# Kernel tuning notes

Hardware: AMD Instinct MI355X
Metric: run time of the kernel (lower is better)

The kernel has to match this reference:

```python
import jax, jax.numpy as jnp
import numpy as np

NUM_HEADS = 8
MODEL_DIM = 1024
SEQ_LEN = 2048


def setup_inputs() -> dict:
    key = jax.random.key(0)
    ks = jax.random.split(key, 9)
    H, D, L = NUM_HEADS, MODEL_DIM, SEQ_LEN
    s_in = 1.0 / np.sqrt(D)
    s_out = 1.0 / np.sqrt(H * D)
    return {
        "tokens": jax.random.normal(ks[0], (D, L), dtype=jnp.float32),
        "Wq": jax.random.uniform(ks[1], (H * D, D), jnp.float32, -s_in, s_in),
        "bq": jax.random.uniform(ks[2], (H * D,), jnp.float32, -s_in, s_in),
        "Wk": jax.random.uniform(ks[3], (H * D, D), jnp.float32, -s_in, s_in),
        "bk": jax.random.uniform(ks[4], (H * D,), jnp.float32, -s_in, s_in),
        "Wv": jax.random.uniform(ks[5], (H * D, D), jnp.float32, -s_in, s_in),
        "bv": jax.random.uniform(ks[6], (H * D,), jnp.float32, -s_in, s_in),
        "Wo": jax.random.uniform(ks[7], (D, H * D), jnp.float32, -s_out, s_out),
        "bo": jax.random.uniform(ks[8], (D,), jnp.float32, -s_out, s_out),
    }


def _split_heads(x, H, D, L):
    # Faithful to torch: raw .view of contiguous [H*D, L] into (L, H, D),
    # then permute(1, 2, 0) -> (H, D, L). This is a memory reinterpretation,
    # not a transpose, exactly as in the original module.
    return x.reshape(L, H, D).transpose(1, 2, 0)


def reference(tokens, Wq, bq, Wk, bk, Wv, bv, Wo, bo):
    D, L = tokens.shape
    H = Wq.shape[0] // D
    # 1x1 Conv1d == matmul over channel dim
    q = _split_heads(Wq @ tokens + bq[:, None], H, D, L)  # (H, D, L)
    k = _split_heads(Wk @ tokens + bk[:, None], H, D, L)  # (H, D, L)
    v = _split_heads(Wv @ tokens + bv[:, None], H, D, L)  # (H, D, L)
    scores = jnp.einsum("hdl,hdm->hlm", q, k) / np.sqrt(D)  # (H, L, L)
    # torch F.softmax without dim on a 3D tensor -> dim=0 (head axis)
    attn = jax.nn.softmax(scores, axis=0)
    ctx = jnp.einsum("hlm,hdm->hdl", attn, v)  # (H, D, L)
    out = Wo @ ctx.reshape(H * D, L) + bo[:, None]  # (D, L)
    return out
```

## Files before the change

kernel.cpp:

```cpp
#include <hip/hip_runtime.h>

#define SEQL 2048
#define DMODEL 1024
#define HDIM 8192

typedef unsigned short bf16_t;
typedef __attribute__((ext_vector_type(8))) short bf16x8;
typedef __attribute__((ext_vector_type(4))) float f32x4;

__device__ __forceinline__ bf16_t f2bf(float f) {
  unsigned u = __float_as_uint(f);
  u += 0x7fffu + ((u >> 16) & 1u);
  return (bf16_t)(u >> 16);
}
__device__ __forceinline__ float bf2f(bf16_t b) {
  return __uint_as_float(((unsigned)b) << 16);
}

__global__ __launch_bounds__(256) void cvt_f32_bf16(const float* __restrict__ in,
                                                    bf16_t* __restrict__ out, int n) {
  int i = (blockIdx.x * 256 + threadIdx.x) * 4;
  if (i >= n) return;
  float4 f = *reinterpret_cast<const float4*>(in + i);
  ushort4 u;
  u.x = f2bf(f.x); u.y = f2bf(f.y); u.z = f2bf(f.z); u.w = f2bf(f.w);
  *reinterpret_cast<ushort4*>(out + i) = u;
}

__global__ __launch_bounds__(256) void transpose_cvt(const float* __restrict__ in,
                                                     bf16_t* __restrict__ out) {
  __shared__ float tile[32][33];
  int bx = blockIdx.x * 32;
  int by = blockIdx.y * 32;
  int tx = threadIdx.x, ty = threadIdx.y;
#pragma unroll
  for (int i = ty; i < 32; i += 8)
    tile[i][tx] = in[(size_t)(by + i) * SEQL + bx + tx];
  __syncthreads();
#pragma unroll
  for (int i = ty; i < 32; i += 8)
    out[(size_t)(bx + i) * DMODEL + by + tx] = f2bf(tile[tx][i]);
}

__global__ __launch_bounds__(256) void softmax_heads(bf16_t* __restrict__ S) {
  const size_t HS = (size_t)SEQL * SEQL;
  size_t p = ((size_t)blockIdx.x * 256 + threadIdx.x) * 8;
  float v[8][8];
#pragma unroll
  for (int h = 0; h < 8; ++h) {
    bf16x8 x = *reinterpret_cast<const bf16x8*>(S + h * HS + p);
#pragma unroll
    for (int e = 0; e < 8; ++e) v[h][e] = bf2f((bf16_t)x[e]);
  }
#pragma unroll
  for (int e = 0; e < 8; ++e) {
    float mx = v[0][e];
#pragma unroll
    for (int h = 1; h < 8; ++h) mx = fmaxf(mx, v[h][e]);
    float s = 0.f;
#pragma unroll
    for (int h = 0; h < 8; ++h) { v[h][e] = __expf(v[h][e] - mx); s += v[h][e]; }
    float inv = 1.0f / s;
#pragma unroll
    for (int h = 0; h < 8; ++h) v[h][e] *= inv;
  }
#pragma unroll
  for (int h = 0; h < 8; ++h) {
    bf16x8 x;
#pragma unroll
    for (int e = 0; e < 8; ++e) x[e] = (short)f2bf(v[h][e]);
    *reinterpret_cast<bf16x8*>(S + h * HS + p) = x;
  }
}

__global__ __launch_bounds__(256) void reduce_out(const float* __restrict__ P,
                                                  const float* __restrict__ bo,
                                                  float* __restrict__ out) {
  const size_t NEL = (size_t)DMODEL * SEQL;
  size_t i = ((size_t)blockIdx.x * 256 + threadIdx.x) * 4;
  float4 a = *reinterpret_cast<const float4*>(P + i);
#pragma unroll
  for (int z = 1; z < 8; ++z) {
    float4 b = *reinterpret_cast<const float4*>(P + z * NEL + i);
    a.x += b.x; a.y += b.y; a.z += b.z; a.w += b.w;
  }
  float bias = bo[i / SEQL];
  a.x += bias; a.y += bias; a.z += bias; a.w += bias;
  *reinterpret_cast<float4*>(out + i) = a;
}

template <typename OutT, int EPI, bool HAS_BIAS>
__global__ __launch_bounds__(512, 2) void gemm256(
    const bf16_t* __restrict__ A, const bf16_t* __restrict__ B,
    OutT* __restrict__ C, const float* __restrict__ bias,
    int M, int N, int K, int lda, int ldb, int ldc,
    long long sA, long long sB, long long sC, float scale, int gx) {
  __shared__ alignas(16) char smem[147456];
  auto* As = reinterpret_cast<bf16_t(*)[2][8192]>(smem);
  auto* Bs = reinterpret_cast<bf16_t(*)[2][8192]>(smem + 65536);
  const int z = blockIdx.z;
  A += (long long)z * sA;
  B += (long long)z * sB;
  C += (long long)z * sC;
  const int nwg = gridDim.x;
  const int bid = blockIdx.x;
  const int swz = (nwg & 7) ? bid : ((bid & 7) * (nwg >> 3) + (bid >> 3));
  const int brow = (swz / gx) * 256;
  const int bcol = (swz % gx) * 256;
  const int tid = threadIdx.x;
  const int w = tid >> 6, lane = tid & 63;
  const int fr = lane & 15, fq = lane >> 4;
  const int wr = w >> 2, wc = w & 3;

  int rj[2], cj[2];
#pragma unroll
  for (int j = 0; j < 2; ++j) {
    const int c = (w * 2 + j) * 64 + lane;
    rj[j] = c >> 3;
    cj[j] = ((c & 7) ^ (rj[j] & 7)) << 3;
  }

  auto stageA = [&](int buf, int half, int kk) {
#pragma unroll
    for (int j = 0; j < 2; ++j) {
      const bf16_t* g = A + (size_t)(brow + half * 128 + rj[j]) * lda + kk + cj[j];
      __builtin_amdgcn_global_load_lds(
          (const __attribute__((address_space(1))) void*)g,
          (__attribute__((address_space(3))) void*)(&As[buf][half][(w * 2 + j) * 512]),
          16, 0, 0);
    }
  };
  auto stageB = [&](int buf, int half, int kk) {
#pragma unroll
    for (int j = 0; j < 2; ++j) {
      const bf16_t* g = B + (size_t)(bcol + half * 128 + rj[j]) * ldb + kk + cj[j];
      __builtin_amdgcn_global_load_lds(
          (const __attribute__((address_space(1))) void*)g,
          (__attribute__((address_space(3))) void*)(&Bs[buf][half][(w * 2 + j) * 512]),
          16, 0, 0);
    }
  };

  auto ldA = [&](int buf, int mf, int kk) -> bf16x8 {
    const int rr = mf * 16 + fr;
    return *reinterpret_cast<const bf16x8*>(
        &As[buf][wr][rr * 64 + ((((kk << 2) | fq) ^ (rr & 7)) << 3)]);
  };
  auto ldB = [&](int buf, int nf, int kk) -> bf16x8 {
    const int rr = (wc & 1) * 64 + nf * 16 + fr;
    return *reinterpret_cast<const bf16x8*>(
        &Bs[buf][wc >> 1][rr * 64 + ((((kk << 2) | fq) ^ (rr & 7)) << 3)]);
  };

  f32x4 acc[8][4];
  const f32x4 fzero = {0.f, 0.f, 0.f, 0.f};
#pragma unroll
  for (int m = 0; m < 8; ++m)
#pragma unroll
    for (int n = 0; n < 4; ++n) acc[m][n] = fzero;

  const int NT = K >> 6;
  stageA(0, 0, 0); stageA(0, 1, 0); stageB(0, 0, 0); stageB(0, 1, 0);
  __syncthreads();

  for (int t = 0; t < NT; ++t) {
    const int p = t & 1, q = p ^ 1;
    const int kn = (t + 1) << 6;
    const bool pre = (t + 1 < NT);
    bf16x8 af[4][2], bg[4][2];

    if (pre) { stageA(q, 0, kn); stageA(q, 1, kn); }
#pragma unroll
    for (int mf = 0; mf < 4; ++mf)
#pragma unroll
      for (int kk = 0; kk < 2; ++kk) af[mf][kk] = ldA(p, mf, kk);
#pragma unroll
    for (int nf = 0; nf < 2; ++nf)
#pragma unroll
      for (int kk = 0; kk < 2; ++kk) bg[nf][kk] = ldB(p, nf, kk);
    __builtin_amdgcn_s_setprio(1);
#pragma unroll
    for (int mf = 0; mf < 4; ++mf)
#pragma unroll
      for (int nf = 0; nf < 2; ++nf)
#pragma unroll
        for (int kk = 0; kk < 2; ++kk)
          acc[mf][nf] = __builtin_amdgcn_mfma_f32_16x16x32_bf16(
              af[mf][kk], bg[nf][kk], acc[mf][nf], 0, 0, 0);
    __builtin_amdgcn_s_setprio(0);

    if (pre) { stageB(q, 0, kn); stageB(q, 1, kn); }
#pragma unroll
    for (int nf = 2; nf < 4; ++nf)
#pragma unroll
      for (int kk = 0; kk < 2; ++kk) bg[nf][kk] = ldB(p, nf, kk);
    __builtin_amdgcn_s_setprio(1);
#pragma unroll
    for (int mf = 0; mf < 4; ++mf)
#pragma unroll
      for (int nf = 2; nf < 4; ++nf)
#pragma unroll
        for (int kk = 0; kk < 2; ++kk)
          acc[mf][nf] = __builtin_amdgcn_mfma_f32_16x16x32_bf16(
              af[mf][kk], bg[nf][kk], acc[mf][nf], 0, 0, 0);
    __builtin_amdgcn_s_setprio(0);

#pragma unroll
    for (int mf = 0; mf < 4; ++mf)
#pragma unroll
      for (int kk = 0; kk < 2; ++kk) af[mf][kk] = ldA(p, mf + 4, kk);
    __builtin_amdgcn_s_setprio(1);
#pragma unroll
    for (int mf = 0; mf < 4; ++mf)
#pragma unroll
      for (int nf = 2; nf < 4; ++nf)
#pragma unroll
        for (int kk = 0; kk < 2; ++kk)
          acc[mf + 4][nf] = __builtin_amdgcn_mfma_f32_16x16x32_bf16(
              af[mf][kk], bg[nf][kk], acc[mf + 4][nf], 0, 0, 0);
    __builtin_amdgcn_s_setprio(0);

#pragma unroll
    for (int nf = 0; nf < 2; ++nf)
#pragma unroll
      for (int kk = 0; kk < 2; ++kk) bg[nf][kk] = ldB(p, nf, kk);
    __builtin_amdgcn_s_setprio(1);
#pragma unroll
    for (int mf = 0; mf < 4; ++mf)
#pragma unroll
      for (int nf = 0; nf < 2; ++nf)
#pragma unroll
        for (int kk = 0; kk < 2; ++kk)
          acc[mf + 4][nf] = __builtin_amdgcn_mfma_f32_16x16x32_bf16(
              af[mf][kk], bg[nf][kk], acc[mf + 4][nf], 0, 0, 0);
    __builtin_amdgcn_s_setprio(0);

    if (pre) __syncthreads();
  }

  __syncthreads();

  if constexpr (EPI == 0) {
    bf16_t* Ct = (bf16_t*)smem;
#pragma unroll
    for (int mf = 0; mf < 8; ++mf)
#pragma unroll
      for (int j = 0; j < 4; ++j) {
        const int orow = wr * 128 + mf * 16 + fq * 4 + j;
        float bvv = HAS_BIAS ? bias[brow + orow] : 0.f;
#pragma unroll
        for (int nf = 0; nf < 4; ++nf)
          Ct[orow * 264 + wc * 64 + nf * 16 + fr] = f2bf(acc[mf][nf][j] * scale + bvv);
      }
    __syncthreads();
#pragma unroll
    for (int i = 0; i < 16; ++i) {
      const int c = tid + i * 512;
      const int row = c >> 5, ch = c & 31;
      *reinterpret_cast<bf16x8*>(&C[(size_t)(brow + row) * ldc + bcol + ch * 8]) =
          *reinterpret_cast<const bf16x8*>(smem + row * 528 + ch * 16);
    }
  } else if constexpr (EPI == 1) {
    float* Cf = (float*)smem;
#pragma unroll
    for (int h = 0; h < 2; ++h) {
      if (wr == h) {
#pragma unroll
        for (int mf = 0; mf < 8; ++mf)
#pragma unroll
          for (int j = 0; j < 4; ++j) {
            const int orow = mf * 16 + fq * 4 + j;
            float bvv = HAS_BIAS ? bias[brow + h * 128 + orow] : 0.f;
#pragma unroll
            for (int nf = 0; nf < 4; ++nf)
              Cf[orow * 264 + wc * 64 + nf * 16 + fr] = acc[mf][nf][j] * scale + bvv;
          }
      }
      __syncthreads();
#pragma unroll
      for (int i = 0; i < 16; ++i) {
        const int c = tid + i * 512;
        const int row = c >> 6, ch = c & 63;
        *reinterpret_cast<float4*>(&C[(size_t)(brow + h * 128 + row) * ldc + bcol + ch * 4]) =
            *reinterpret_cast<const float4*>(smem + row * 1056 + ch * 16);
      }
      __syncthreads();
    }
  } else {
    bf16_t* Vt = (bf16_t*)smem;
#pragma unroll
    for (int mf = 0; mf < 8; ++mf)
#pragma unroll
      for (int j = 0; j < 4; ++j) {
        const int i = wr * 128 + mf * 16 + fq * 4 + j;
        const int mloc = i >> 2;
        float bvv = HAS_BIAS ? bias[brow + i] : 0.f;
#pragma unroll
        for (int nf = 0; nf < 4; ++nf) {
          const int dloc = wc * 64 + nf * 16 + fr;
          Vt[(j * 256 + dloc) * 72 + mloc] = f2bf(acc[mf][nf][j] * scale + bvv);
        }
      }
    __syncthreads();
    const int r_ = bcol >> 10, d0 = bcol & 1023, m0 = brow >> 2;
#pragma unroll
    for (int sIt = 0; sIt < 2; ++sIt) {
      const int s = tid + sIt * 512;
      const int h2 = s >> 8, dloc = s & 255;
      const bf16_t* src = Vt + (h2 * 256 + dloc) * 72;
      bf16_t* dst = (bf16_t*)C + ((size_t)(2 * h2 + r_) * DMODEL + d0 + dloc) * SEQL + m0;
#pragma unroll
      for (int qq = 0; qq < 8; ++qq)
        *reinterpret_cast<bf16x8*>(dst + qq * 8) =
            *reinterpret_cast<const bf16x8*>(src + qq * 8);
    }
  }
}

extern "C" void kernel_launch(void* const* d_in, const int* in_sizes, int n_in,
                              void* d_out, int out_size, void* d_ws, size_t ws_size,
                              hipStream_t stream) {
  const float* tokens = (const float*)d_in[0];
  const float* Wq = (const float*)d_in[1];
  const float* bq = (const float*)d_in[2];
  const float* Wk = (const float*)d_in[3];
  const float* bk = (const float*)d_in[4];
  const float* Wv = (const float*)d_in[5];
  const float* bv = (const float*)d_in[6];
  const float* Wo = (const float*)d_in[7];
  const float* bo = (const float*)d_in[8];
  float* out = (float*)d_out;
  char* ws = (char*)d_ws;
  const size_t MB = 1024ull * 1024ull;
  bf16_t* tT = (bf16_t*)(ws + 0);
  bf16_t* Wb = (bf16_t*)(ws + 4 * MB);
  bf16_t* Qm = (bf16_t*)(ws + 20 * MB);
  bf16_t* Km = (bf16_t*)(ws + 52 * MB);
  bf16_t* Vs = (bf16_t*)(ws + 84 * MB);
  bf16_t* Sb = (bf16_t*)(ws + 116 * MB);
  bf16_t* cT = (bf16_t*)(ws + 20 * MB);
  float* Pp = (float*)(ws + 116 * MB);

  dim3 b256(256);
  dim3 b512(512);
  const int nW = HDIM * DMODEL;

  transpose_cvt<<<dim3(SEQL / 32, DMODEL / 32), dim3(32, 8), 0, stream>>>(tokens, tT);

  cvt_f32_bf16<<<nW / 1024, b256, 0, stream>>>(Wq, Wb, nW);
  gemm256<bf16_t, 0, true><<<dim3(32 * 8, 1, 1), b512, 0, stream>>>(
      Wb, tT, Qm, bq, HDIM, SEQL, DMODEL, DMODEL, DMODEL, SEQL, 0, 0, 0, 1.0f, 8);
  cvt_f32_bf16<<<nW / 1024, b256, 0, stream>>>(Wk, Wb, nW);
  gemm256<bf16_t, 0, true><<<dim3(32 * 8, 1, 1), b512, 0, stream>>>(
      Wb, tT, Km, bk, HDIM, SEQL, DMODEL, DMODEL, DMODEL, SEQL, 0, 0, 0, 1.0f, 8);
  cvt_f32_bf16<<<nW / 1024, b256, 0, stream>>>(Wv, Wb, nW);
  gemm256<bf16_t, 2, true><<<dim3(32 * 8, 1, 1), b512, 0, stream>>>(
      Wb, tT, Vs, bv, HDIM, SEQL, DMODEL, DMODEL, DMODEL, SEQL, 0, 0, 0, 1.0f, 8);

  gemm256<bf16_t, 0, false><<<dim3(8 * 8, 1, 8), b512, 0, stream>>>(
      Qm, Km, Sb, nullptr, SEQL, SEQL, DMODEL, HDIM, HDIM, SEQL,
      1024, 1024, (long long)SEQL * SEQL, 0.03125f, 8);

  softmax_heads<<<(SEQL * SEQL / 8) / 256, b256, 0, stream>>>(Sb);

  gemm256<bf16_t, 0, false><<<dim3(8 * 4, 1, 8), b512, 0, stream>>>(
      Sb, Vs, cT, nullptr, SEQL, DMODEL, SEQL, SEQL, SEQL, HDIM,
      (long long)SEQL * SEQL, (long long)DMODEL * SEQL, DMODEL, 1.0f, 4);

  cvt_f32_bf16<<<nW / 1024, b256, 0, stream>>>(Wo, Wb, nW);
  gemm256<float, 1, false><<<dim3(4 * 8, 1, 8), b512, 0, stream>>>(
      Wb, cT, Pp, nullptr, DMODEL, SEQL, 1024, HDIM, HDIM, SEQL,
      1024, 1024, (long long)DMODEL * SEQL, 1.0f, 8);
  reduce_out<<<(DMODEL * SEQL / 4) / 256, b256, 0, stream>>>(Pp, bo, out);
}
```

Measured before the change: 369.2 us.

## Fuse Q/K/V projections into one GEMM and flatten batched grids

Converts Wq, Wk and Wv into one concatenated bf16 weight buffer and runs a single 768-tile GEMM that writes Q and K row-major and V in its transposed-split layout, chosen per tile. All batched GEMMs now fold the batch index into a flat 1D grid, so the XCD swizzle covers every tile instead of only one z-slice. The intent is to cut launch count, fill the GPU better with more tiles per launch, and reduce per-launch tail effects. The cost is larger workspace and a runtime branch in the epilogue.

```diff
diff --git a/kernel.cpp b/kernel.cpp
--- a/kernel.cpp
+++ b/kernel.cpp
@@ -27,6 +27,32 @@
   *reinterpret_cast<ushort4*>(out + i) = u;
 }
 
+__global__ __launch_bounds__(256) void cvt3_f32_bf16(const float* __restrict__ a,
+                                                     const float* __restrict__ b,
+                                                     const float* __restrict__ c,
+                                                     bf16_t* __restrict__ out) {
+  const int SEG = HDIM * DMODEL;
+  int i = (blockIdx.x * 256 + threadIdx.x) * 4;
+  const float* src;
+  int off;
+  if (i < SEG) { src = a; off = i; }
+  else if (i < 2 * SEG) { src = b; off = i - SEG; }
+  else { src = c; off = i - 2 * SEG; }
+  float4 f = *reinterpret_cast<const float4*>(src + off);
+  ushort4 u;
+  u.x = f2bf(f.x); u.y = f2bf(f.y); u.z = f2bf(f.z); u.w = f2bf(f.w);
+  *reinterpret_cast<ushort4*>(out + i) = u;
+}
+
+__global__ __launch_bounds__(256) void bias3(const float* __restrict__ a,
+                                             const float* __restrict__ b,
+                                             const float* __restrict__ c,
+                                             float* __restrict__ out) {
+  int i = blockIdx.x * 256 + threadIdx.x;
+  float v = (i < HDIM) ? a[i] : (i < 2 * HDIM) ? b[i - HDIM] : c[i - 2 * HDIM];
+  out[i] = v;
+}
+
 __global__ __launch_bounds__(256) void transpose_cvt(const float* __restrict__ in,
                                                      bf16_t* __restrict__ out) {
   __shared__ float tile[32][33];
@@ -92,21 +118,22 @@
 template <typename OutT, int EPI, bool HAS_BIAS>
 __global__ __launch_bounds__(512, 2) void gemm256(
     const bf16_t* __restrict__ A, const bf16_t* __restrict__ B,
-    OutT* __restrict__ C, const float* __restrict__ bias,
-    int M, int N, int K, int lda, int ldb, int ldc,
-    long long sA, long long sB, long long sC, float scale, int gx) {
+    OutT* __restrict__ C, bf16_t* __restrict__ C2, const float* __restrict__ bias,
+    int K, int lda, int ldb, int ldc,
+    long long sA, long long sB, long long sC, float scale, int gx, int gxy) {
   __shared__ alignas(16) char smem[147456];
   auto* As = reinterpret_cast<bf16_t(*)[2][8192]>(smem);
   auto* Bs = reinterpret_cast<bf16_t(*)[2][8192]>(smem + 65536);
-  const int z = blockIdx.z;
-  A += (long long)z * sA;
-  B += (long long)z * sB;
-  C += (long long)z * sC;
   const int nwg = gridDim.x;
   const int bid = blockIdx.x;
   const int swz = (nwg & 7) ? bid : ((bid & 7) * (nwg >> 3) + (bid >> 3));
-  const int brow = (swz / gx) * 256;
-  const int bcol = (swz % gx) * 256;
+  const int zz = swz / gxy;
+  const int rem = swz - zz * gxy;
+  const int brow = (rem / gx) * 256;
+  const int bcol = (rem % gx) * 256;
+  A += (long long)zz * sA;
+  B += (long long)zz * sB;
+  C += (long long)zz * sC;
   const int tid = threadIdx.x;
   const int w = tid >> 6, lane = tid & 63;
   const int fr = lane & 15, fq = lane >> 4;
@@ -240,7 +267,8 @@
 
   __syncthreads();
 
-  if constexpr (EPI == 0) {
+  const bool vseg = (EPI == 2) && (brow >= 2 * HDIM);
+  if ((EPI == 0) || ((EPI == 2) && !vseg)) {
     bf16_t* Ct = (bf16_t*)smem;
 #pragma unroll
     for (int mf = 0; mf < 8; ++mf)
@@ -253,11 +281,12 @@
           Ct[orow * 264 + wc * 64 + nf * 16 + fr] = f2bf(acc[mf][nf][j] * scale + bvv);
       }
     __syncthreads();
+    bf16_t* Cb = (bf16_t*)C;
 #pragma unroll
     for (int i = 0; i < 16; ++i) {
       const int c = tid + i * 512;
       const int row = c >> 5, ch = c & 31;
-      *reinterpret_cast<bf16x8*>(&C[(size_t)(brow + row) * ldc + bcol + ch * 8]) =
+      *reinterpret_cast<bf16x8*>(&Cb[(size_t)(brow + row) * ldc + bcol + ch * 8]) =
           *reinterpret_cast<const bf16x8*>(smem + row * 528 + ch * 16);
     }
   } else if constexpr (EPI == 1) {
@@ -286,7 +315,8 @@
       }
       __syncthreads();
     }
-  } else {
+  } else if constexpr (EPI == 2) {
+    const int vrow = brow - 2 * HDIM;
     bf16_t* Vt = (bf16_t*)smem;
 #pragma unroll
     for (int mf = 0; mf < 8; ++mf)
@@ -302,13 +332,13 @@
         }
       }
     __syncthreads();
-    const int r_ = bcol >> 10, d0 = bcol & 1023, m0 = brow >> 2;
+    const int r_ = bcol >> 10, d0 = bcol & 1023, m0 = vrow >> 2;
 #pragma unroll
     for (int sIt = 0; sIt < 2; ++sIt) {
       const int s = tid + sIt * 512;
       const int h2 = s >> 8, dloc = s & 255;
       const bf16_t* src = Vt + (h2 * 256 + dloc) * 72;
-      bf16_t* dst = (bf16_t*)C + ((size_t)(2 * h2 + r_) * DMODEL + d0 + dloc) * SEQL + m0;
+      bf16_t* dst = C2 + ((size_t)(2 * h2 + r_) * DMODEL + d0 + dloc) * SEQL + m0;
 #pragma unroll
       for (int qq = 0; qq < 8; ++qq)
         *reinterpret_cast<bf16x8*>(dst + qq * 8) =
@@ -332,44 +362,43 @@
   float* out = (float*)d_out;
   char* ws = (char*)d_ws;
   const size_t MB = 1024ull * 1024ull;
-  bf16_t* tT = (bf16_t*)(ws + 0);
-  bf16_t* Wb = (bf16_t*)(ws + 4 * MB);
-  bf16_t* Qm = (bf16_t*)(ws + 20 * MB);
-  bf16_t* Km = (bf16_t*)(ws + 52 * MB);
-  bf16_t* Vs = (bf16_t*)(ws + 84 * MB);
-  bf16_t* Sb = (bf16_t*)(ws + 116 * MB);
-  bf16_t* cT = (bf16_t*)(ws + 20 * MB);
-  float* Pp = (float*)(ws + 116 * MB);
+  bf16_t* Vs = (bf16_t*)(ws + 0);
+  bf16_t* QmKm = (bf16_t*)(ws + 32 * MB);
+  bf16_t* Qm = QmKm;
+  bf16_t* Km = QmKm + (size_t)HDIM * SEQL;
+  bf16_t* Sb = (bf16_t*)(ws + 96 * MB);
+  bf16_t* tT = (bf16_t*)(ws + 96 * MB);
+  bf16_t* Wqkv = (bf16_t*)(ws + 100 * MB);
+  float* bqkv = (float*)(ws + 148 * MB);
+  bf16_t* cT = (bf16_t*)(ws + 32 * MB);
+  bf16_t* Wob = (bf16_t*)(ws + 64 * MB);
+  float* Pp = (float*)(ws + 96 * MB);
 
   dim3 b256(256);
   dim3 b512(512);
   const int nW = HDIM * DMODEL;
 
   transpose_cvt<<<dim3(SEQL / 32, DMODEL / 32), dim3(32, 8), 0, stream>>>(tokens, tT);
-
-  cvt_f32_bf16<<<nW / 1024, b256, 0, stream>>>(Wq, Wb, nW);
-  gemm256<bf16_t, 0, true><<<dim3(32 * 8, 1, 1), b512, 0, stream>>>(
-      Wb, tT, Qm, bq, HDIM, SEQL, DMODEL, DMODEL, DMODEL, SEQL, 0, 0, 0, 1.0f, 8);
-  cvt_f32_bf16<<<nW / 1024, b256, 0, stream>>>(Wk, Wb, nW);
-  gemm256<bf16_t, 0, true><<<dim3(32 * 8, 1, 1), b512, 0, stream>>>(
-      Wb, tT, Km, bk, HDIM, SEQL, DMODEL, DMODEL, DMODEL, SEQL, 0, 0, 0, 1.0f, 8);
-  cvt_f32_bf16<<<nW / 1024, b256, 0, stream>>>(Wv, Wb, nW);
-  gemm256<bf16_t, 2, true><<<dim3(32 * 8, 1, 1), b512, 0, stream>>>(
-      Wb, tT, Vs, bv, HDIM, SEQL, DMODEL, DMODEL, DMODEL, SEQL, 0, 0, 0, 1.0f, 8);
-
-  gemm256<bf16_t, 0, false><<<dim3(8 * 8, 1, 8), b512, 0, stream>>>(
-      Qm, Km, Sb, nullptr, SEQL, SEQL, DMODEL, HDIM, HDIM, SEQL,
-      1024, 1024, (long long)SEQL * SEQL, 0.03125f, 8);
+  cvt3_f32_bf16<<<3 * nW / 1024, b256, 0, stream>>>(Wq, Wk, Wv, Wqkv);
+  bias3<<<3 * HDIM / 256, b256, 0, stream>>>(bq, bk, bv, bqkv);
+
+  gemm256<bf16_t, 2, true><<<dim3(768, 1, 1), b512, 0, stream>>>(
+      Wqkv, tT, QmKm, Vs, bqkv, DMODEL, DMODEL, DMODEL, SEQL,
+      0, 0, 0, 1.0f, 8, 768);
+
+  gemm256<bf16_t, 0, false><<<dim3(512, 1, 1), b512, 0, stream>>>(
+      Qm, Km, Sb, nullptr, nullptr, DMODEL, HDIM, HDIM, SEQL,
+      1024, 1024, (long long)SEQL * SEQL, 0.03125f, 8, 64);
 
   softmax_heads<<<(SEQL * SEQL / 8) / 256, b256, 0, stream>>>(Sb);
 
-  gemm256<bf16_t, 0, false><<<dim3(8 * 4, 1, 8), b512, 0, stream>>>(
-      Sb, Vs, cT, nullptr, SEQL, DMODEL, SEQL, SEQL, SEQL, HDIM,
-      (long long)SEQL * SEQL, (long long)DMODEL * SEQL, DMODEL, 1.0f, 4);
-
-  cvt_f32_bf16<<<nW / 1024, b256, 0, stream>>>(Wo, Wb, nW);
-  gemm256<float, 1, false><<<dim3(4 * 8, 1, 8), b512, 0, stream>>>(
-      Wb, cT, Pp, nullptr, DMODEL, SEQL, 1024, HDIM, HDIM, SEQL,
-      1024, 1024, (long long)DMODEL * SEQL, 1.0f, 8);
+  gemm256<bf16_t, 0, false><<<dim3(256, 1, 1), b512, 0, stream>>>(
+      Sb, Vs, cT, nullptr, nullptr, SEQL, SEQL, SEQL, HDIM,
+      (long long)SEQL * SEQL, (long long)DMODEL * SEQL, 1024, 1.0f, 4, 32);
+
+  cvt_f32_bf16<<<nW / 1024, b256, 0, stream>>>(Wo, Wob, nW);
+  gemm256<float, 1, false><<<dim3(256, 1, 1), b512, 0, stream>>>(
+      Wob, cT, Pp, nullptr, nullptr, 1024, HDIM, HDIM, SEQL,
+      1024, 1024, (long long)DMODEL * SEQL, 1.0f, 8, 32);
   reduce_out<<<(DMODEL * SEQL / 4) / 256, b256, 0, stream>>>(Pp, bo, out);
 }
```

New measurement: 366.6 us. No clear change (-0.7%).
